# Kernel optimization log

Measured on AMD Instinct MI355X. Metric: run time of the kernel, lower is better.

## Reference

```python
import jax, jax.numpy as jnp
import numpy as np

EMBED_DIM = 768


def setup_inputs() -> dict:
    key = jax.random.key(0)
    k1, k2, k3, k4, k5 = jax.random.split(key, 5)
    C = EMBED_DIM
    B, N = 32, 1024
    s = 1.0 / np.sqrt(C)
    x = jax.random.normal(k1, (B, N, C), dtype=jnp.float32)
    qkv_w = jax.random.normal(k2, (C, 3 * C), dtype=jnp.float32) * s  # [in, out]
    qkv_b = jax.random.normal(k3, (3 * C,), dtype=jnp.float32) * 0.02
    proj_w = jax.random.normal(k4, (C, C), dtype=jnp.float32) * s
    proj_b = jax.random.normal(k5, (C,), dtype=jnp.float32) * 0.02
    return {"x": x, "qkv_w": qkv_w, "qkv_b": qkv_b, "proj_w": proj_w, "proj_b": proj_b}


def reference(x, qkv_w, qkv_b, proj_w, proj_b):
    B, N, C = x.shape
    qkv = (x @ qkv_w + qkv_b).reshape(B, N, 3, C)
    q, k, v = qkv[:, :, 0], qkv[:, :, 1], qkv[:, :, 2]  # each [B, N, C]
    # single-head full attention; scale by sqrt(C) as in source
    scores = jnp.einsum('bnc,bmc->bnm', q, k) / jnp.sqrt(jnp.asarray(C, x.dtype))
    attn = jax.nn.softmax(scores, axis=-1)  # dropout p=0.0 -> identity
    out = jnp.einsum('bnm,bmc->bnc', attn, v)
    # faithful to source: transpose(1,2).reshape(B,N,C) permutes the data
    out = jnp.swapaxes(out, 1, 2).reshape(B, N, C)
    return out @ proj_w + proj_b
```

## Files before the change

### kernel.cpp

```cpp
#include <hip/hip_runtime.h>
#include <hip/hip_bf16.h>


#define BM 256
#define BN 256
#define BKK 64

typedef __attribute__((ext_vector_type(8))) short bf16x8;
typedef __attribute__((ext_vector_type(4))) float f32x4;

__device__ __forceinline__ unsigned short f2b(float f) {
  unsigned int u = __float_as_uint(f);
  u = u + 0x7fffu + ((u >> 16) & 1u);
  return (unsigned short)(u >> 16);
}

__device__ __forceinline__ void g2l16(const void* g, void* l) {
  __builtin_amdgcn_global_load_lds(
      (const __attribute__((address_space(1))) unsigned int*)g,
      (__attribute__((address_space(3))) unsigned int*)l, 16, 0, 0);
}

template <int EPI, int SWAP>
__global__ __launch_bounds__(512, 2) void gemm_nt8(
    const unsigned short* __restrict__ A, const unsigned short* __restrict__ B,
    unsigned short* __restrict__ Cb, unsigned short* __restrict__ Ck,
    unsigned short* __restrict__ Cv, float* __restrict__ Cf,
    const float* __restrict__ bias, float* __restrict__ Z, int K, int lda,
    int ldb, int ldc, long bsA, long bsB, long bsC, float scale) {
  __shared__ unsigned short As[2][BM][BKK];
  __shared__ unsigned short Bs[2][BN][BKK];

  const int bxn = SWAP ? blockIdx.y : blockIdx.x;
  const int bym = SWAP ? blockIdx.x : blockIdx.y;
  const int bz = blockIdx.z;
  const unsigned short* Ag = A + (long)bz * bsA + (long)(bym * BM) * lda;
  const unsigned short* Bg = B + (long)bz * bsB + (long)(bxn * BN) * ldb;

  const int tid = threadIdx.x;
  const int wave = tid >> 6;
  const int lane = tid & 63;
  const int l15 = lane & 15;
  const int lk = lane >> 4;
  const int wm = (wave >> 2) << 7;
  const int wn = (wave & 3) << 6;

  const int sr = lane >> 3;
  const int sc = (lane & 7) ^ sr;

  f32x4 acc[8][4];
#pragma unroll
  for (int m = 0; m < 8; ++m)
#pragma unroll
    for (int n = 0; n < 4; ++n)
#pragma unroll
      for (int p = 0; p < 4; ++p) acc[m][n][p] = 0.f;

  auto stA = [&](int d, int h, int k0) {
#pragma unroll
    for (int i = 0; i < 2; ++i) {
      const int rb = (h << 7) + (wave << 4) + (i << 3);
      g2l16(Ag + (long)(rb + sr) * lda + k0 + (sc << 3), &As[d][rb][0]);
    }
  };
  auto stB = [&](int d, int h, int k0) {
#pragma unroll
    for (int i = 0; i < 2; ++i) {
      const int rb = (h << 7) + (wave << 4) + (i << 3);
      g2l16(Bg + (long)(rb + sr) * ldb + k0 + (sc << 3), &Bs[d][rb][0]);
    }
  };
  auto ldA = [&](int d, int m, int ks) {
    return *(const bf16x8*)&As[d][wm + (m << 4) + l15]
                              [((((ks << 2) | lk) ^ (l15 & 7)) << 3)];
  };
  auto ldB = [&](int d, int n, int ks) {
    return *(const bf16x8*)&Bs[d][wn + (n << 4) + l15]
                              [((((ks << 2) | lk) ^ (l15 & 7)) << 3)];
  };

  const int NT = K / BKK;
  stA(0, 0, 0); stA(0, 1, 0); stB(0, 0, 0); stB(0, 1, 0);
  stA(1, 0, BKK); stA(1, 1, BKK); stB(1, 0, BKK); stB(1, 1, BKK);
  asm volatile("s_waitcnt vmcnt(8)" ::: "memory");
  __builtin_amdgcn_sched_barrier(0);
  __builtin_amdgcn_s_barrier();

  int cur = 0;
  for (int t = 0; t < NT; ++t) {
    const int nxt = cur ^ 1;
    const bool st = (t >= 1) && (t + 1 < NT);
    const int k1 = (t + 1) * BKK;

    bf16x8 aL[4][2], bA[2][2];
#pragma unroll
    for (int m = 0; m < 4; ++m)
#pragma unroll
      for (int ks = 0; ks < 2; ++ks) aL[m][ks] = ldA(cur, m, ks);
#pragma unroll
    for (int n = 0; n < 2; ++n)
#pragma unroll
      for (int ks = 0; ks < 2; ++ks) bA[n][ks] = ldB(cur, n, ks);
    if (st) { stA(nxt, 0, k1); stA(nxt, 1, k1); }
    __builtin_amdgcn_s_barrier();
    asm volatile("s_waitcnt lgkmcnt(0)" ::: "memory");
    __builtin_amdgcn_sched_barrier(0);
    __builtin_amdgcn_s_setprio(1);
#pragma unroll
    for (int m = 0; m < 4; ++m)
#pragma unroll
      for (int n = 0; n < 2; ++n)
#pragma unroll
        for (int ks = 0; ks < 2; ++ks)
          acc[m][n] = __builtin_amdgcn_mfma_f32_16x16x32_bf16(
              aL[m][ks], bA[n][ks], acc[m][n], 0, 0, 0);
    __builtin_amdgcn_s_setprio(0);
    __builtin_amdgcn_s_barrier();

    bf16x8 bB[2][2];
#pragma unroll
    for (int n = 0; n < 2; ++n)
#pragma unroll
      for (int ks = 0; ks < 2; ++ks) bB[n][ks] = ldB(cur, n + 2, ks);
    if (st) { stB(nxt, 0, k1); stB(nxt, 1, k1); }
    __builtin_amdgcn_s_barrier();
    asm volatile("s_waitcnt lgkmcnt(0)" ::: "memory");
    __builtin_amdgcn_sched_barrier(0);
    __builtin_amdgcn_s_setprio(1);
#pragma unroll
    for (int m = 0; m < 4; ++m)
#pragma unroll
      for (int n = 0; n < 2; ++n)
#pragma unroll
        for (int ks = 0; ks < 2; ++ks)
          acc[m][n + 2] = __builtin_amdgcn_mfma_f32_16x16x32_bf16(
              aL[m][ks], bB[n][ks], acc[m][n + 2], 0, 0, 0);
    __builtin_amdgcn_s_setprio(0);
    __builtin_amdgcn_s_barrier();

    bf16x8 aH[4][2];
#pragma unroll
    for (int m = 0; m < 4; ++m)
#pragma unroll
      for (int ks = 0; ks < 2; ++ks) aH[m][ks] = ldA(cur, m + 4, ks);
    __builtin_amdgcn_s_barrier();
    asm volatile("s_waitcnt lgkmcnt(0)" ::: "memory");
    __builtin_amdgcn_sched_barrier(0);
    __builtin_amdgcn_s_setprio(1);
#pragma unroll
    for (int m = 0; m < 4; ++m)
#pragma unroll
      for (int n = 0; n < 2; ++n)
#pragma unroll
        for (int ks = 0; ks < 2; ++ks)
          acc[m + 4][n] = __builtin_amdgcn_mfma_f32_16x16x32_bf16(
              aH[m][ks], bA[n][ks], acc[m + 4][n], 0, 0, 0);
    __builtin_amdgcn_s_setprio(0);
    __builtin_amdgcn_s_barrier();

    __builtin_amdgcn_s_setprio(1);
#pragma unroll
    for (int m = 0; m < 4; ++m)
#pragma unroll
      for (int n = 0; n < 2; ++n)
#pragma unroll
        for (int ks = 0; ks < 2; ++ks)
          acc[m + 4][n + 2] = __builtin_amdgcn_mfma_f32_16x16x32_bf16(
              aH[m][ks], bB[n][ks], acc[m + 4][n + 2], 0, 0, 0);
    __builtin_amdgcn_s_setprio(0);
    __syncthreads();
    cur = nxt;
  }

  const int row0 = bym * BM + wm + (lk << 2);
  const int col0 = bxn * BN + wn;

  if constexpr (EPI == 1) {
    const int seg = (bxn * BN) / 768;
    unsigned short* O = (seg == 0) ? Cb : ((seg == 1) ? Ck : Cv);
#pragma unroll
    for (int n = 0; n < 4; ++n) {
      const int col = col0 + (n << 4) + l15;
      const float bv = bias[col];
      const int cl = col - seg * 768;
#pragma unroll
      for (int m = 0; m < 8; ++m)
#pragma unroll
        for (int p = 0; p < 4; ++p)
          O[(long)(row0 + (m << 4) + p) * 768 + cl] = f2b(acc[m][n][p] + bv);
    }
  } else if constexpr (EPI == 2) {
#pragma unroll
    for (int n = 0; n < 4; ++n) {
      const int col = col0 + (n << 4) + l15;
      const float bv = bias[col];
#pragma unroll
      for (int m = 0; m < 8; ++m)
#pragma unroll
        for (int p = 0; p < 4; ++p)
          Cf[(long)(row0 + (m << 4) + p) * ldc + col] = acc[m][n][p] + bv;
    }
  } else if constexpr (EPI == 3) {
    unsigned short* C = Cb + (long)bz * bsC;
#pragma unroll
    for (int m = 0; m < 8; ++m) {
      float es[4] = {0.f, 0.f, 0.f, 0.f};
#pragma unroll
      for (int n = 0; n < 4; ++n) {
        const int col = col0 + (n << 4) + l15;
#pragma unroll
        for (int p = 0; p < 4; ++p) {
          const float e = __expf(acc[m][n][p] * scale);
          es[p] += e;
          C[(long)(row0 + (m << 4) + p) * ldc + col] = f2b(e);
        }
      }
#pragma unroll
      for (int p = 0; p < 4; ++p) {
        float s = es[p];
        s += __shfl_xor(s, 1);
        s += __shfl_xor(s, 2);
        s += __shfl_xor(s, 4);
        s += __shfl_xor(s, 8);
        if (l15 == 0)
          atomicAdd(&Z[(long)bz * 1024 + row0 + (m << 4) + p], s);
      }
    }
  } else {
    unsigned short* C = Cb + (long)bz * bsC;
#pragma unroll
    for (int n = 0; n < 4; ++n) {
      const int col = col0 + (n << 4) + l15;
      const float zinv = 1.f / Z[(long)bz * 1024 + col];
#pragma unroll
      for (int m = 0; m < 8; ++m)
#pragma unroll
        for (int p = 0; p < 4; ++p)
          C[(long)(row0 + (m << 4) + p) * ldc + col] =
              f2b(acc[m][n][p] * zinv);
    }
  }
}

__global__ __launch_bounds__(256) void prep(
    const float4* __restrict__ x, ushort4* __restrict__ x_bf,
    const float* __restrict__ qkv_w, unsigned short* __restrict__ Wqkv,
    const float* __restrict__ proj_w, unsigned short* __restrict__ Wp) {
  const int blk = blockIdx.x;
  if (blk < 24576) {
    const long i = (long)blk * 256 + threadIdx.x;
    float4 f = x[i];
    ushort4 o;
    o.x = f2b(f.x); o.y = f2b(f.y); o.z = f2b(f.z); o.w = f2b(f.w);
    x_bf[i] = o;
  } else if (blk < 24576 + 6912) {
    const long i = (long)(blk - 24576) * 256 + threadIdx.x;
    const int k = (int)(i % 768);
    const int j = (int)(i / 768);
    Wqkv[i] = f2b(qkv_w[(long)k * 2304 + j]);
  } else {
    const long i = (long)(blk - 24576 - 6912) * 256 + threadIdx.x;
    const int k = (int)(i % 768);
    const int j = (int)(i / 768);
    Wp[i] = f2b(proj_w[(long)k * 768 + j]);
  }
}

__global__ __launch_bounds__(256) void transpose_v(
    const unsigned short* __restrict__ V, unsigned short* __restrict__ Vt) {
  __shared__ unsigned short T[64][72];
  const int b = blockIdx.z;
  const int d0 = blockIdx.x << 6;
  const int m0 = blockIdx.y << 6;
  const unsigned short* Vb = V + (long)b * 786432;
  unsigned short* Vtb = Vt + (long)b * 786432;
  const int tid = threadIdx.x;
  const int r = tid >> 2;
  const int c4 = tid & 3;
#pragma unroll
  for (int h = 0; h < 2; ++h) {
    const int cc = (c4 + (h << 2)) << 3;
    *(uint4*)&T[r][cc] = *(const uint4*)&Vb[(long)(m0 + r) * 768 + d0 + cc];
  }
  __syncthreads();
#pragma unroll
  for (int h = 0; h < 2; ++h) {
    const int mm = (c4 + (h << 2)) << 3;
    alignas(16) unsigned short tmp[8];
#pragma unroll
    for (int e = 0; e < 8; ++e) tmp[e] = T[mm + e][r];
    *(uint4*)&Vtb[(long)(d0 + r) * 1024 + m0 + mm] = *(uint4*)tmp;
  }
}

extern "C" void kernel_launch(void* const* d_in, const int* in_sizes, int n_in,
                              void* d_out, int out_size, void* d_ws,
                              size_t ws_size, hipStream_t stream) {
  const float* x = (const float*)d_in[0];
  const float* qkv_w = (const float*)d_in[1];
  const float* qkv_b = (const float*)d_in[2];
  const float* proj_w = (const float*)d_in[3];
  const float* proj_b = (const float*)d_in[4];
  float* out = (float*)d_out;

  char* ws = (char*)d_ws;
  unsigned short* x_bf = (unsigned short*)ws;
  unsigned short* Wqkv = (unsigned short*)(ws + 50331648);
  unsigned short* Wp = (unsigned short*)(ws + 53870592);
  unsigned short* Qb = (unsigned short*)(ws + 55050240);
  unsigned short* Kb = (unsigned short*)(ws + 105381888);
  unsigned short* Vb = (unsigned short*)(ws + 155713536);
  unsigned short* Sb = (unsigned short*)(ws + 206045184);
  unsigned short* Vt = x_bf;
  unsigned short* Hb = Qb;
  float* Zs = (float*)Vb;

  prep<<<33792, 256, 0, stream>>>((const float4*)x, (ushort4*)x_bf, qkv_w,
                                  Wqkv, proj_w, Wp);

  gemm_nt8<1, 1><<<dim3(128, 9, 1), 512, 0, stream>>>(
      x_bf, Wqkv, Qb, Kb, Vb, nullptr, qkv_b, nullptr, 768, 768, 768, 0, 0, 0,
      0, 1.f);

  transpose_v<<<dim3(12, 16, 32), 256, 0, stream>>>(Vb, Vt);

  hipMemsetAsync(Zs, 0, 32 * 1024 * sizeof(float), stream);

  gemm_nt8<3, 0><<<dim3(4, 4, 32), 512, 0, stream>>>(
      Qb, Kb, Sb, nullptr, nullptr, nullptr, nullptr, Zs, 768, 768, 768, 1024,
      786432, 786432, 1048576, 0.03608439182435161f);

  gemm_nt8<4, 0><<<dim3(4, 3, 32), 512, 0, stream>>>(
      Vt, Sb, Hb, nullptr, nullptr, nullptr, nullptr, Zs, 1024, 1024, 1024,
      1024, 786432, 1048576, 786432, 1.f);

  gemm_nt8<2, 1><<<dim3(128, 3, 1), 512, 0, stream>>>(
      Hb, Wp, nullptr, nullptr, nullptr, out, proj_b, nullptr, 768, 768, 768,
      768, 0, 0, 0, 1.f);
}
```

Measured before the change: 588.5 us.

## Prefetch K-tiles two stages ahead and reorder epilogue stores by row

The main loop now issues global-to-LDS loads for tile t+2 into the buffer just consumed, placed after that buffer's last reads. It replaces the full __syncthreads with a partial vmcnt wait plus a barrier, so loads stay in flight across iterations. The epilogues hoist the bias and 1/Z loads and loop over rows outermost, so consecutive stores hit the same row. The deeper prefetch depends on the vmcnt count matching the number of outstanding loads, and overwriting the current buffer relies on the barrier placement being correct.

Result: faster. 553.8 us (-5.9%).

```diff
diff --git a/kernel.cpp b/kernel.cpp
--- a/kernel.cpp
+++ b/kernel.cpp
@@ -89,8 +89,8 @@
   int cur = 0;
   for (int t = 0; t < NT; ++t) {
     const int nxt = cur ^ 1;
-    const bool st = (t >= 1) && (t + 1 < NT);
-    const int k1 = (t + 1) * BKK;
+    const bool st2 = (t + 2 < NT);
+    const int k2 = (t + 2) * BKK;
 
     bf16x8 aL[4][2], bA[2][2];
 #pragma unroll
@@ -101,7 +101,6 @@
     for (int n = 0; n < 2; ++n)
 #pragma unroll
       for (int ks = 0; ks < 2; ++ks) bA[n][ks] = ldB(cur, n, ks);
-    if (st) { stA(nxt, 0, k1); stA(nxt, 1, k1); }
     __builtin_amdgcn_s_barrier();
     asm volatile("s_waitcnt lgkmcnt(0)" ::: "memory");
     __builtin_amdgcn_sched_barrier(0);
@@ -122,7 +121,6 @@
     for (int n = 0; n < 2; ++n)
 #pragma unroll
       for (int ks = 0; ks < 2; ++ks) bB[n][ks] = ldB(cur, n + 2, ks);
-    if (st) { stB(nxt, 0, k1); stB(nxt, 1, k1); }
     __builtin_amdgcn_s_barrier();
     asm volatile("s_waitcnt lgkmcnt(0)" ::: "memory");
     __builtin_amdgcn_sched_barrier(0);
@@ -143,6 +141,7 @@
     for (int m = 0; m < 4; ++m)
 #pragma unroll
       for (int ks = 0; ks < 2; ++ks) aH[m][ks] = ldA(cur, m + 4, ks);
+    if (st2) { stB(cur, 0, k2); stB(cur, 1, k2); }
     __builtin_amdgcn_s_barrier();
     asm volatile("s_waitcnt lgkmcnt(0)" ::: "memory");
     __builtin_amdgcn_sched_barrier(0);
@@ -158,6 +157,7 @@
     __builtin_amdgcn_s_setprio(0);
     __builtin_amdgcn_s_barrier();
 
+    if (st2) { stA(cur, 0, k2); stA(cur, 1, k2); }
     __builtin_amdgcn_s_setprio(1);
 #pragma unroll
     for (int m = 0; m < 4; ++m)
@@ -168,7 +168,12 @@
           acc[m + 4][n + 2] = __builtin_amdgcn_mfma_f32_16x16x32_bf16(
               aH[m][ks], bB[n][ks], acc[m + 4][n + 2], 0, 0, 0);
     __builtin_amdgcn_s_setprio(0);
-    __syncthreads();
+    if (st2)
+      asm volatile("s_waitcnt vmcnt(8)" ::: "memory");
+    else
+      asm volatile("s_waitcnt vmcnt(0)" ::: "memory");
+    __builtin_amdgcn_sched_barrier(0);
+    __builtin_amdgcn_s_barrier();
     cur = nxt;
   }
 
@@ -178,41 +183,45 @@
   if constexpr (EPI == 1) {
     const int seg = (bxn * BN) / 768;
     unsigned short* O = (seg == 0) ? Cb : ((seg == 1) ? Ck : Cv);
-#pragma unroll
-    for (int n = 0; n < 4; ++n) {
-      const int col = col0 + (n << 4) + l15;
-      const float bv = bias[col];
-      const int cl = col - seg * 768;
-#pragma unroll
-      for (int m = 0; m < 8; ++m)
-#pragma unroll
-        for (int p = 0; p < 4; ++p)
-          O[(long)(row0 + (m << 4) + p) * 768 + cl] = f2b(acc[m][n][p] + bv);
-    }
+    float bv[4];
+#pragma unroll
+    for (int n = 0; n < 4; ++n) bv[n] = bias[col0 + (n << 4) + l15];
+    const int cl0 = col0 + l15 - seg * 768;
+#pragma unroll
+    for (int m = 0; m < 8; ++m)
+#pragma unroll
+      for (int p = 0; p < 4; ++p) {
+        const long rr = row0 + (m << 4) + p;
+#pragma unroll
+        for (int n = 0; n < 4; ++n)
+          O[rr * 768 + cl0 + (n << 4)] = f2b(acc[m][n][p] + bv[n]);
+      }
   } else if constexpr (EPI == 2) {
-#pragma unroll
-    for (int n = 0; n < 4; ++n) {
-      const int col = col0 + (n << 4) + l15;
-      const float bv = bias[col];
-#pragma unroll
-      for (int m = 0; m < 8; ++m)
-#pragma unroll
-        for (int p = 0; p < 4; ++p)
-          Cf[(long)(row0 + (m << 4) + p) * ldc + col] = acc[m][n][p] + bv;
-    }
+    float bv[4];
+#pragma unroll
+    for (int n = 0; n < 4; ++n) bv[n] = bias[col0 + (n << 4) + l15];
+#pragma unroll
+    for (int m = 0; m < 8; ++m)
+#pragma unroll
+      for (int p = 0; p < 4; ++p) {
+        const long rr = row0 + (m << 4) + p;
+#pragma unroll
+        for (int n = 0; n < 4; ++n)
+          Cf[rr * ldc + col0 + (n << 4) + l15] = acc[m][n][p] + bv[n];
+      }
   } else if constexpr (EPI == 3) {
     unsigned short* C = Cb + (long)bz * bsC;
 #pragma unroll
     for (int m = 0; m < 8; ++m) {
       float es[4] = {0.f, 0.f, 0.f, 0.f};
 #pragma unroll
-      for (int n = 0; n < 4; ++n) {
-        const int col = col0 + (n << 4) + l15;
-#pragma unroll
-        for (int p = 0; p < 4; ++p) {
+      for (int p = 0; p < 4; ++p) {
+        const long rr = row0 + (m << 4) + p;
+#pragma unroll
+        for (int n = 0; n < 4; ++n) {
           const float e = __expf(acc[m][n][p] * scale);
           es[p] += e;
-          C[(long)(row0 + (m << 4) + p) * ldc + col] = f2b(e);
+          C[rr * ldc + col0 + (n << 4) + l15] = f2b(e);
         }
       }
 #pragma unroll
@@ -228,17 +237,19 @@
     }
   } else {
     unsigned short* C = Cb + (long)bz * bsC;
-#pragma unroll
-    for (int n = 0; n < 4; ++n) {
-      const int col = col0 + (n << 4) + l15;
-      const float zinv = 1.f / Z[(long)bz * 1024 + col];
-#pragma unroll
-      for (int m = 0; m < 8; ++m)
-#pragma unroll
-        for (int p = 0; p < 4; ++p)
-          C[(long)(row0 + (m << 4) + p) * ldc + col] =
-              f2b(acc[m][n][p] * zinv);
-    }
+    float zv[4];
+#pragma unroll
+    for (int n = 0; n < 4; ++n)
+      zv[n] = 1.f / Z[(long)bz * 1024 + col0 + (n << 4) + l15];
+#pragma unroll
+    for (int m = 0; m < 8; ++m)
+#pragma unroll
+      for (int p = 0; p < 4; ++p) {
+        const long rr = row0 + (m << 4) + p;
+#pragma unroll
+        for (int n = 0; n < 4; ++n)
+          C[rr * ldc + col0 + (n << 4) + l15] = f2b(acc[m][n][p] * zv[n]);
+      }
   }
 }
 
```
